# Performance work log

Hardware: AMD Instinct MI355X
Metric: run time of the kernel (lower is better)

Reference implementation:

```python
import jax, jax.numpy as jnp
import numpy as np

ED = 200      # entity/relation dim
KW = 9        # kernel width
OC = 32       # out channels
WOUT = ED - KW + 1  # 192 valid-conv output width
B = 1024
NE = 40943
NR = 18


def setup_inputs() -> dict:
    key = jax.random.key(0)
    ks = jax.random.split(key, 9)
    g = lambda k, shape: jax.random.normal(k, shape, jnp.float32) * 0.05
    return dict(
        e1_idx=jax.random.randint(ks[0], (B,), 0, NE, dtype=jnp.int32),
        r_idx=jax.random.randint(ks[1], (B,), 0, NR, dtype=jnp.int32),
        W1=g(ks[2], (ED, KW * OC)),
        b1=g(ks[3], (KW * OC,)),
        W2=g(ks[4], (WOUT * OC, ED)),
        b2=g(ks[5], (ED,)),
        bias_logits=g(ks[6], (NE,)),
        E=g(ks[7], (NE, ED)),
        R=g(ks[8], (NR, ED)),
    )


def reference(e1_idx, r_idx, W1, b1, W2, b2, bias_logits, E, R):
    e1 = E[e1_idx]          # [B, 200]
    r = R[r_idx]            # [B, 200]
    # hypernetwork: relation -> per-sample conv filters [B, KW, OC]
    k = (r @ W1 + b1).reshape(-1, KW, OC)
    # per-sample valid 1D conv of e1 with its own filters (depthwise-as-groups trick collapsed)
    idx = jnp.arange(WOUT)[:, None] + jnp.arange(KW)[None, :]  # [WOUT, KW]
    patches = e1[:, idx]                                        # [B, WOUT, KW]
    # flatten order matches TF: (out_channel major, width minor)
    feat = jnp.einsum('bwj,bjo->bow', patches, k).reshape(e1.shape[0], OC * WOUT)
    h = jax.nn.relu(feat @ W2 + b2)                             # [B, 200]
    logits = h @ E.T + bias_logits                              # [B, NE]
    return logits
```

## Files before the change

### kernel.cpp

```cpp
#include <hip/hip_runtime.h>

#define NE 40943
#define NR 18
#define ED 200
#define KWC 9
#define OC 32
#define WOUT 192
#define KOC 288
#define KH 224
#define G2_LD 40

typedef unsigned short u16;
typedef unsigned int u32;
typedef __bf16 bf16x8 __attribute__((ext_vector_type(8)));
typedef float f32x4 __attribute__((ext_vector_type(4)));
typedef u16 u16x8 __attribute__((ext_vector_type(8)));
typedef u16 u16x4 __attribute__((ext_vector_type(4)));

__device__ __forceinline__ u16 f2bf(float f) {
  u32 u = __builtin_bit_cast(u32, f);
  u32 r = (u + 0x7fffu + ((u >> 16) & 1u)) >> 16;
  return (u16)r;
}

__global__ void prep_k_kernel(const float* __restrict__ R,
                              const float* __restrict__ W1,
                              const float* __restrict__ b1,
                              float* __restrict__ KrT) {
  int rel = blockIdx.x;
  int j = threadIdx.x;
  float acc = b1[j];
  const float* rrow = R + rel * ED;
  for (int d = 0; d < ED; ++d) acc += rrow[d] * W1[d * KOC + j];
  KrT[j * NR + rel] = acc;
}

__global__ __launch_bounds__(256) void build_c_kernel(const float* __restrict__ KrT,
                                                      const float* __restrict__ W2,
                                                      float* __restrict__ C) {
  int p = blockIdx.x;
  int d = threadIdx.x;
  int jlo = p > (WOUT - 1) ? p - (WOUT - 1) : 0;
  int jhi = p < (KWC - 1) ? p : (KWC - 1);
  if (d < ED) {
    float acc[NR];
#pragma unroll
    for (int r = 0; r < NR; ++r) acc[r] = 0.f;
    for (int j = jlo; j <= jhi; ++j) {
      int w = p - j;
      const float* w2base = W2 + (size_t)w * ED + d;
      const float* kb = KrT + (j * OC) * NR;
#pragma unroll
      for (int o = 0; o < OC; ++o) {
        float w2v = w2base[(size_t)o * WOUT * ED];
#pragma unroll
        for (int r = 0; r < NR; ++r) acc[r] += kb[o * NR + r] * w2v;
      }
    }
#pragma unroll
    for (int r = 0; r < NR; ++r) C[((size_t)r * ED + p) * ED + d] = acc[r];
  }
}

__global__ __launch_bounds__(256) void h_kernel(const int* __restrict__ e1_idx,
                                                const int* __restrict__ r_idx,
                                                const float* __restrict__ E,
                                                const float* __restrict__ C,
                                                const float* __restrict__ b2,
                                                u16* __restrict__ Hb) {
  __shared__ float e1s[ED];
  int b = blockIdx.x;
  int t = threadIdx.x;
  if (t < ED) e1s[t] = E[(size_t)e1_idx[b] * ED + t];
  __syncthreads();
  int r = r_idx[b];
  const float* Cr = C + (size_t)r * ED * ED;
  if (t < KH) {
    float acc = 0.f;
    if (t < ED) {
#pragma unroll 8
      for (int p = 0; p < ED; ++p) acc += e1s[p] * Cr[(size_t)p * ED + t];
      acc += b2[t];
      acc = acc > 0.f ? acc : 0.f;
    }
    Hb[(size_t)b * KH + t] = (t < ED) ? f2bf(acc) : (u16)0;
  }
}

__global__ void conv_e_kernel(const float* __restrict__ E, u16* __restrict__ Eb) {
  int idx = blockIdx.x * 256 + threadIdx.x;
  const int total = NE * (KH / 4);
  if (idx >= total) return;
  int row = idx / (KH / 4);
  int c4 = (idx % (KH / 4)) * 4;
  u16x4 st = {0, 0, 0, 0};
  if (c4 < ED) {
    f32x4 v = *(const f32x4*)(E + (size_t)row * ED + c4);
    st[0] = f2bf(v[0]); st[1] = f2bf(v[1]); st[2] = f2bf(v[2]); st[3] = f2bf(v[3]);
  }
  *(u16x4*)(Eb + (size_t)row * KH + c4) = st;
}

__global__ __launch_bounds__(256) void gemm2_kernel(
    const u16* __restrict__ Hb,
    const u16* __restrict__ Eb,
    const float* __restrict__ bias,
    float* __restrict__ out) {
  __shared__ u16 lA[128 * G2_LD];
  __shared__ u16 lB[128 * G2_LD];
  const int t = threadIdx.x;
  const int m0 = blockIdx.y * 128;
  const int n0 = blockIdx.x * 128;
  const int wave = t >> 6, lane = t & 63;
  const int wm = (wave >> 1) * 64, wn = (wave & 1) * 64;
  const int lr = lane & 15, lq = lane >> 4;
  f32x4 zero = {0.f, 0.f, 0.f, 0.f};
  f32x4 acc[4][4];
#pragma unroll
  for (int i = 0; i < 4; ++i)
#pragma unroll
    for (int j = 0; j < 4; ++j) acc[i][j] = zero;

  for (int k0 = 0; k0 < KH; k0 += 32) {
#pragma unroll
    for (int s = 0; s < 2; ++s) {
      int v = t + s * 256;
      int r = v >> 2;
      int c8 = (v & 3) * 8;
      *(u16x8*)(lA + r * G2_LD + c8) = *(const u16x8*)(Hb + (size_t)(m0 + r) * KH + k0 + c8);
      int gr = n0 + r;
      u16x8 bv = {0, 0, 0, 0, 0, 0, 0, 0};
      if (gr < NE) bv = *(const u16x8*)(Eb + (size_t)gr * KH + k0 + c8);
      *(u16x8*)(lB + r * G2_LD + c8) = bv;
    }
    __syncthreads();
    bf16x8 af[4], bfv[4];
#pragma unroll
    for (int mi = 0; mi < 4; ++mi)
      af[mi] = *(const bf16x8*)(lA + (wm + mi * 16 + lr) * G2_LD + lq * 8);
#pragma unroll
    for (int ni = 0; ni < 4; ++ni)
      bfv[ni] = *(const bf16x8*)(lB + (wn + ni * 16 + lr) * G2_LD + lq * 8);
#pragma unroll
    for (int mi = 0; mi < 4; ++mi)
#pragma unroll
      for (int ni = 0; ni < 4; ++ni)
        acc[mi][ni] = __builtin_amdgcn_mfma_f32_16x16x32_bf16(af[mi], bfv[ni], acc[mi][ni], 0, 0, 0);
    __syncthreads();
  }
#pragma unroll
  for (int mi = 0; mi < 4; ++mi) {
    int row = m0 + wm + mi * 16 + lq * 4;
#pragma unroll
    for (int ni = 0; ni < 4; ++ni) {
      int col = n0 + wn + ni * 16 + lr;
      if (col < NE) {
        float bv = bias[col];
#pragma unroll
        for (int i = 0; i < 4; ++i)
          out[(size_t)(row + i) * NE + col] = acc[mi][ni][i] + bv;
      }
    }
  }
}

extern "C" void kernel_launch(void* const* d_in, const int* in_sizes, int n_in,
                              void* d_out, int out_size, void* d_ws, size_t ws_size,
                              hipStream_t stream) {
  const int* e1_idx = (const int*)d_in[0];
  const int* r_idx = (const int*)d_in[1];
  const float* W1 = (const float*)d_in[2];
  const float* b1 = (const float*)d_in[3];
  const float* W2 = (const float*)d_in[4];
  const float* b2 = (const float*)d_in[5];
  const float* bias_logits = (const float*)d_in[6];
  const float* E = (const float*)d_in[7];
  const float* R = (const float*)d_in[8];
  float* out = (float*)d_out;

  char* ws = (char*)d_ws;
  float* KrT = (float*)ws;
  float* C = (float*)(ws + 32768);
  u16* Hb = (u16*)(ws + 32768 + 2880000);
  u16* Eb = (u16*)(ws + 32768 + 2880000 + 458752);

  prep_k_kernel<<<dim3(NR), dim3(KOC), 0, stream>>>(R, W1, b1, KrT);
  build_c_kernel<<<dim3(ED), dim3(256), 0, stream>>>(KrT, W2, C);
  h_kernel<<<dim3(1024), dim3(256), 0, stream>>>(e1_idx, r_idx, E, C, b2, Hb);
  conv_e_kernel<<<dim3((NE * (KH / 4) + 255) / 256), dim3(256), 0, stream>>>(E, Eb);
  gemm2_kernel<<<dim3((NE + 127) / 128, 8), dim3(256), 0, stream>>>(Hb, Eb, bias_logits, out);
}
```

Measured before the change: 319.6 us.

## Double-buffer GEMM tiles via direct global-to-LDS loads with swizzle and XCD remap

The logits GEMM now loads its A and B tiles straight into LDS with global_load_lds, replacing the register round trip. It double-buffers those tiles so the next K-slice is fetched while MFMAs run on the current one. An XOR swizzle on the 32-wide rows replaces the padded layout to avoid LDS bank conflicts. The grid is flattened and remapped so each XCD gets a contiguous range of N-tiles, which should improve L2 reuse. Out-of-range B rows are clamped rather than zero-filled, which relies on the final column mask for correctness.

```diff
diff --git a/kernel.cpp b/kernel.cpp
--- a/kernel.cpp
+++ b/kernel.cpp
@@ -8,7 +8,6 @@
 #define WOUT 192
 #define KOC 288
 #define KH 224
-#define G2_LD 40
 
 typedef unsigned short u16;
 typedef unsigned int u32;
@@ -21,6 +20,12 @@
   u32 u = __builtin_bit_cast(u32, f);
   u32 r = (u + 0x7fffu + ((u >> 16) & 1u)) >> 16;
   return (u16)r;
+}
+
+__device__ __forceinline__ void gl_lds16(const u16* g, u16* l) {
+  __builtin_amdgcn_global_load_lds(
+      (const __attribute__((address_space(1))) u32*)g,
+      (__attribute__((address_space(3))) u32*)l, 16, 0, 0);
 }
 
 __global__ void prep_k_kernel(const float* __restrict__ R,
@@ -106,14 +111,35 @@
     const u16* __restrict__ Eb,
     const float* __restrict__ bias,
     float* __restrict__ out) {
-  __shared__ u16 lA[128 * G2_LD];
-  __shared__ u16 lB[128 * G2_LD];
+  __shared__ __align__(16) u16 lA[2][128 * 32];
+  __shared__ __align__(16) u16 lB[2][128 * 32];
   const int t = threadIdx.x;
-  const int m0 = blockIdx.y * 128;
-  const int n0 = blockIdx.x * 128;
   const int wave = t >> 6, lane = t & 63;
+
+  int id = blockIdx.x;
+  int xcd = id & 7;
+  int q = id >> 3;
+  int bx = xcd * 40 + q % 40;
+  int by = q / 40;
+  const int m0 = by * 128;
+  const int n0 = bx * 128;
   const int wm = (wave >> 1) * 64, wn = (wave & 1) * 64;
   const int lr = lane & 15, lq = lane >> 4;
+  const int csw = (lq ^ ((lr >> 1) & 3)) * 8;
+
+  int aoff[2], boff[2], loff[2];
+#pragma unroll
+  for (int s = 0; s < 2; ++s) {
+    int chunk = wave * 128 + s * 64 + lane;
+    int r = chunk >> 2, cc = chunk & 3;
+    int ccs = cc ^ ((r >> 1) & 3);
+    loff[s] = chunk * 8;
+    aoff[s] = (m0 + r) * KH + ccs * 8;
+    int gr = n0 + r;
+    if (gr > NE - 1) gr = NE - 1;
+    boff[s] = gr * KH + ccs * 8;
+  }
+
   f32x4 zero = {0.f, 0.f, 0.f, 0.f};
   f32x4 acc[4][4];
 #pragma unroll
@@ -121,33 +147,43 @@
 #pragma unroll
     for (int j = 0; j < 4; ++j) acc[i][j] = zero;
 
-  for (int k0 = 0; k0 < KH; k0 += 32) {
-#pragma unroll
-    for (int s = 0; s < 2; ++s) {
-      int v = t + s * 256;
-      int r = v >> 2;
-      int c8 = (v & 3) * 8;
-      *(u16x8*)(lA + r * G2_LD + c8) = *(const u16x8*)(Hb + (size_t)(m0 + r) * KH + k0 + c8);
-      int gr = n0 + r;
-      u16x8 bv = {0, 0, 0, 0, 0, 0, 0, 0};
-      if (gr < NE) bv = *(const u16x8*)(Eb + (size_t)gr * KH + k0 + c8);
-      *(u16x8*)(lB + r * G2_LD + c8) = bv;
-    }
-    __syncthreads();
+#pragma unroll
+  for (int s = 0; s < 2; ++s) {
+    gl_lds16(Hb + aoff[s], &lA[0][loff[s]]);
+    gl_lds16(Eb + boff[s], &lB[0][loff[s]]);
+  }
+  __syncthreads();
+
+  int cur = 0;
+  for (int kt = 0; kt < KH / 32; ++kt) {
+    if (kt < KH / 32 - 1) {
+      int k0 = (kt + 1) * 32;
+#pragma unroll
+      for (int s = 0; s < 2; ++s) {
+        gl_lds16(Hb + aoff[s] + k0, &lA[cur ^ 1][loff[s]]);
+        gl_lds16(Eb + boff[s] + k0, &lB[cur ^ 1][loff[s]]);
+      }
+    }
     bf16x8 af[4], bfv[4];
 #pragma unroll
-    for (int mi = 0; mi < 4; ++mi)
-      af[mi] = *(const bf16x8*)(lA + (wm + mi * 16 + lr) * G2_LD + lq * 8);
-#pragma unroll
-    for (int ni = 0; ni < 4; ++ni)
-      bfv[ni] = *(const bf16x8*)(lB + (wn + ni * 16 + lr) * G2_LD + lq * 8);
+    for (int mi = 0; mi < 4; ++mi) {
+      int rr = wm + mi * 16 + lr;
+      af[mi] = *(const bf16x8*)(&lA[cur][rr * 32 + csw]);
+    }
+#pragma unroll
+    for (int ni = 0; ni < 4; ++ni) {
+      int rr = wn + ni * 16 + lr;
+      bfv[ni] = *(const bf16x8*)(&lB[cur][rr * 32 + csw]);
+    }
 #pragma unroll
     for (int mi = 0; mi < 4; ++mi)
 #pragma unroll
       for (int ni = 0; ni < 4; ++ni)
         acc[mi][ni] = __builtin_amdgcn_mfma_f32_16x16x32_bf16(af[mi], bfv[ni], acc[mi][ni], 0, 0, 0);
     __syncthreads();
-  }
+    cur ^= 1;
+  }
+
 #pragma unroll
   for (int mi = 0; mi < 4; ++mi) {
     int row = m0 + wm + mi * 16 + lq * 4;
@@ -188,5 +224,5 @@
   build_c_kernel<<<dim3(ED), dim3(256), 0, stream>>>(KrT, W2, C);
   h_kernel<<<dim3(1024), dim3(256), 0, stream>>>(e1_idx, r_idx, E, C, b2, Hb);
   conv_e_kernel<<<dim3((NE * (KH / 4) + 255) / 256), dim3(256), 0, stream>>>(E, Eb);
-  gemm2_kernel<<<dim3((NE + 127) / 128, 8), dim3(256), 0, stream>>>(Hb, Eb, bias_logits, out);
-}
+  gemm2_kernel<<<dim3(320 * 8), dim3(256), 0, stream>>>(Hb, Eb, bias_logits, out);
+}
```

New measurement: 309.5 us. 1.03x faster.

## Load GEMM fragments directly from global memory and remap blocks per XCD

Applied to the files above, without the earlier changes.

The logits GEMM no longer stages A and B tiles through LDS with barriers; each wave loads its MFMA operand fragments straight from global memory, with the whole K loop unrolled. Blocks are linearised and remapped so that consecutive column tiles land on the same XCD, which should improve L2 reuse of the E and H rows. Launch bounds request higher occupancy. The risk is redundant global loads across waves and less coalesced 16-byte row-strided access in exchange for removing LDS traffic and synchronisation.

```diff
diff --git a/kernel.cpp b/kernel.cpp
--- a/kernel.cpp
+++ b/kernel.cpp
@@ -8,7 +8,6 @@
 #define WOUT 192
 #define KOC 288
 #define KH 224
-#define G2_LD 40
 
 typedef unsigned short u16;
 typedef unsigned int u32;
@@ -101,19 +100,36 @@
   *(u16x4*)(Eb + (size_t)row * KH + c4) = st;
 }
 
-__global__ __launch_bounds__(256) void gemm2_kernel(
+__global__ __launch_bounds__(256, 4) void gemm2_kernel(
     const u16* __restrict__ Hb,
     const u16* __restrict__ Eb,
     const float* __restrict__ bias,
     float* __restrict__ out) {
-  __shared__ u16 lA[128 * G2_LD];
-  __shared__ u16 lB[128 * G2_LD];
   const int t = threadIdx.x;
-  const int m0 = blockIdx.y * 128;
-  const int n0 = blockIdx.x * 128;
   const int wave = t >> 6, lane = t & 63;
+
+  int id = blockIdx.x;
+  int xcd = id & 7;
+  int q = id >> 3;
+  int bx = xcd * 40 + q % 40;
+  int by = q / 40;
+  const int m0 = by * 128;
+  const int n0 = bx * 128;
   const int wm = (wave >> 1) * 64, wn = (wave & 1) * 64;
   const int lr = lane & 15, lq = lane >> 4;
+
+  const u16* arow[4];
+  const u16* brow[4];
+#pragma unroll
+  for (int mi = 0; mi < 4; ++mi)
+    arow[mi] = Hb + (size_t)(m0 + wm + mi * 16 + lr) * KH + lq * 8;
+#pragma unroll
+  for (int ni = 0; ni < 4; ++ni) {
+    int gr = n0 + wn + ni * 16 + lr;
+    if (gr > NE - 1) gr = NE - 1;
+    brow[ni] = Eb + (size_t)gr * KH + lq * 8;
+  }
+
   f32x4 zero = {0.f, 0.f, 0.f, 0.f};
   f32x4 acc[4][4];
 #pragma unroll
@@ -121,33 +137,22 @@
 #pragma unroll
     for (int j = 0; j < 4; ++j) acc[i][j] = zero;
 
-  for (int k0 = 0; k0 < KH; k0 += 32) {
 #pragma unroll
-    for (int s = 0; s < 2; ++s) {
-      int v = t + s * 256;
-      int r = v >> 2;
-      int c8 = (v & 3) * 8;
-      *(u16x8*)(lA + r * G2_LD + c8) = *(const u16x8*)(Hb + (size_t)(m0 + r) * KH + k0 + c8);
-      int gr = n0 + r;
-      u16x8 bv = {0, 0, 0, 0, 0, 0, 0, 0};
-      if (gr < NE) bv = *(const u16x8*)(Eb + (size_t)gr * KH + k0 + c8);
-      *(u16x8*)(lB + r * G2_LD + c8) = bv;
-    }
-    __syncthreads();
+  for (int kt = 0; kt < KH / 32; ++kt) {
     bf16x8 af[4], bfv[4];
 #pragma unroll
     for (int mi = 0; mi < 4; ++mi)
-      af[mi] = *(const bf16x8*)(lA + (wm + mi * 16 + lr) * G2_LD + lq * 8);
+      af[mi] = *(const bf16x8*)(arow[mi] + kt * 32);
 #pragma unroll
     for (int ni = 0; ni < 4; ++ni)
-      bfv[ni] = *(const bf16x8*)(lB + (wn + ni * 16 + lr) * G2_LD + lq * 8);
+      bfv[ni] = *(const bf16x8*)(brow[ni] + kt * 32);
 #pragma unroll
     for (int mi = 0; mi < 4; ++mi)
 #pragma unroll
       for (int ni = 0; ni < 4; ++ni)
         acc[mi][ni] = __builtin_amdgcn_mfma_f32_16x16x32_bf16(af[mi], bfv[ni], acc[mi][ni], 0, 0, 0);
-    __syncthreads();
   }
+
 #pragma unroll
   for (int mi = 0; mi < 4; ++mi) {
     int row = m0 + wm + mi * 16 + lq * 4;
@@ -188,5 +193,5 @@
   build_c_kernel<<<dim3(ED), dim3(256), 0, stream>>>(KrT, W2, C);
   h_kernel<<<dim3(1024), dim3(256), 0, stream>>>(e1_idx, r_idx, E, C, b2, Hb);
   conv_e_kernel<<<dim3((NE * (KH / 4) + 255) / 256), dim3(256), 0, stream>>>(E, Eb);
-  gemm2_kernel<<<dim3((NE + 127) / 128, 8), dim3(256), 0, stream>>>(Hb, Eb, bias_logits, out);
+  gemm2_kernel<<<dim3(320 * 8), dim3(256), 0, stream>>>(Hb, Eb, bias_logits, out);
 }
```

Result: no change. 321.9 us (+0.7%).
